# Performance work log

Hardware: AMD Instinct MI355X
Metric: run time of the kernel (lower is better)

Reference implementation:

```python
import jax, jax.numpy as jnp
import numpy as np
import math

L, Bt, IN, H = 512, 128, 512, 60


def setup_inputs() -> dict:
    key = jax.random.key(0)
    k1, k2, k3 = jax.random.split(key, 3)
    inp = jax.random.normal(k1, (L, Bt, IN), dtype=jnp.float32)
    W = jax.random.normal(k2, (H, IN), dtype=jnp.float32) / np.sqrt(IN)
    b = jnp.zeros((H,), dtype=jnp.float32)
    alphabet = jax.random.uniform(k3, (H, 3), dtype=jnp.float32, minval=-math.pi, maxval=math.pi)
    bond_lengths = jnp.array([132.868, 145.801, 152.326], dtype=jnp.float32)
    bond_angles = jnp.array([2.028, 2.124, 1.941], dtype=jnp.float32)
    return {"inp": inp, "W": W, "b": b, "alphabet": alphabet,
            "bond_lengths": bond_lengths, "bond_angles": bond_angles}


def reference(inp, W, b, alphabet, bond_lengths, bond_angles):
    Lr, Bb = inp.shape[0], inp.shape[1]
    # mixture over alphabet of torsion angles
    x = jax.nn.softmax(inp @ W.T + b, axis=2)                 # (L, B, H)
    phi = jnp.arctan2(x @ jnp.sin(alphabet), x @ jnp.cos(alphabet))  # (L, B, 3)
    # per residue i the loop consumes phi[i].T -> bond index is fastest axis
    phi_f = phi.transpose(0, 2, 1).reshape(Lr * 3, Bb)        # (3L, B)
    r = jnp.tile(bond_lengths, Lr)[:, None]                   # (3L, 1)
    th = jnp.tile(bond_angles, Lr)[:, None]                   # (3L, 1)
    # SRF coordinates of every new atom
    c_tilde = jnp.stack([
        (r * jnp.cos(th)) * jnp.ones_like(phi_f),
        r * jnp.cos(phi_f) * jnp.sin(th),
        r * jnp.sin(phi_f) * jnp.sin(th),
    ], axis=-1)                                               # (3L, B, 3)

    e = jnp.eye(3, dtype=inp.dtype)
    carry0 = (jnp.broadcast_to(e[0], (Bb, 3)),
              jnp.broadcast_to(e[1], (Bb, 3)),
              jnp.broadcast_to(e[2], (Bb, 3)))

    def step(carry, ct):
        A, Bp, C = carry                                      # each (B, 3)
        BC = C - Bp
        bc = BC / jnp.linalg.norm(BC, axis=1, keepdims=True)
        AB = Bp - A
        Nv = jnp.cross(AB, bc)
        n = Nv / jnp.linalg.norm(Nv, axis=1, keepdims=True)
        # D = C + R @ c_tilde, R columns = [bc, n x bc, n]
        D = C + bc * ct[:, 0:1] + jnp.cross(n, bc) * ct[:, 1:2] + n * ct[:, 2:3]
        return (Bp, C, D), D

    _, coords = jax.lax.scan(step, carry0, c_tilde)           # (3L, B, 3)
    return coords
```

## Files before the change

kernel.cpp:

```cpp
#include <hip/hip_runtime.h>
#include <math.h>

#define LSEQ  512
#define BT    128
#define INF   512
#define HH    60
#define NSTEP 1536
#define CH2   6

#define MTILE 64
#define KSTG  128
#define BROW  136

typedef __attribute__((ext_vector_type(8))) short bf16x8;
typedef __attribute__((ext_vector_type(4))) float floatx4;

__device__ __forceinline__ unsigned cvt_pk_bf16(float lo, float hi) {
  unsigned r;
  asm("v_cvt_pk_bf16_f32 %0, %1, %2" : "=v"(r) : "v"(lo), "v"(hi));
  return r;
}
__device__ __forceinline__ void split_pair(float a0, float a1,
                                           unsigned& hw, unsigned& lw) {
  hw = cvt_pk_bf16(a0, a1);
  float h0 = __uint_as_float(hw << 16);
  float h1 = __uint_as_float(hw & 0xFFFF0000u);
  lw = cvt_pk_bf16(a0 - h0, a1 - h1);
}

#define GLOAD(dst, ptr, voff) \
  asm volatile("global_load_dwordx4 %0, %1, %2" \
               : "=v"(dst) : "v"(voff), "s"(ptr))

#define WAIT_VM(n) \
  do { asm volatile("s_waitcnt vmcnt(" #n ")" ::: "memory"); \
       __builtin_amdgcn_sched_barrier(0); } while (0)

#define BARRIER() \
  do { asm volatile("s_waitcnt lgkmcnt(0)" ::: "memory"); \
       __builtin_amdgcn_s_barrier(); \
       asm volatile("" ::: "memory"); } while (0)


#define ISSUE_A(BUF, KB) \
  { _Pragma("unroll") \
    for (int ks_ = 0; ks_ < 4; ++ks_) { \
      GLOAD(BUF[2*ks_],   aBase + (KB) + ks_*32,     voffA); \
      GLOAD(BUF[2*ks_+1], aBase + (KB) + ks_*32 + 4, voffA); } }

#define ISSUE_W(KB) \
  { _Pragma("unroll") \
    for (int i_ = 0; i_ < 7; ++i_) \
      GLOAD(Wb[i_], W + (KB) + i_*4096, voffW); \
    GLOAD(Wb[7], W + (KB) + 7*4096, voffWc); }

#define SPLIT_W() \
  { _Pragma("unroll") \
    for (int i_ = 0; i_ < 8; ++i_) { \
      const int chunk_ = i_ * 256 + tid; \
      const int r_  = chunk_ >> 5; \
      const int j4_ = (chunk_ & 31) * 4; \
      floatx4 wv_ = Wb[i_]; \
      if (i_ == 7 && tid >= 128) wv_ = (floatx4){0.f, 0.f, 0.f, 0.f}; \
      unsigned h01_, l01_, h23_, l23_; \
      split_pair(wv_[0], wv_[1], h01_, l01_); \
      split_pair(wv_[2], wv_[3], h23_, l23_); \
      *(uint2*)&BhL[r_ * BROW + j4_] = make_uint2(h01_, h23_); \
      *(uint2*)&BlL[r_ * BROW + j4_] = make_uint2(l01_, l23_); } }

#define DO_STEPS(BUF) \
  { _Pragma("unroll") \
    for (int ks_ = 0; ks_ < 4; ++ks_) { \
      const int kl_ = ks_ * 32; \
      floatx4 x_ = BUF[2*ks_], y_ = BUF[2*ks_+1]; \
      uint4 uh_, ul_; \
      split_pair(x_[0], x_[1], uh_.x, ul_.x); \
      split_pair(x_[2], x_[3], uh_.y, ul_.y); \
      split_pair(y_[0], y_[1], uh_.z, ul_.z); \
      split_pair(y_[2], y_[3], uh_.w, ul_.w); \
      bf16x8 Ah_ = __builtin_bit_cast(bf16x8, uh_); \
      bf16x8 Al_ = __builtin_bit_cast(bf16x8, ul_); \
      _Pragma("unroll") \
      for (int nt_ = 0; nt_ < 4; ++nt_) { \
        const int boff_ = (nt_ * 16 + c) * BROW + kl_ + quad * 8; \
        bf16x8 Bh_ = *(const bf16x8*)&BhL[boff_]; \
        bf16x8 Bl_ = *(const bf16x8*)&BlL[boff_]; \
        acc[nt_] = __builtin_amdgcn_mfma_f32_16x16x32_bf16(Ah_, Bh_, acc[nt_], 0, 0, 0); \
        acc[nt_] = __builtin_amdgcn_mfma_f32_16x16x32_bf16(Ah_, Bl_, acc[nt_], 0, 0, 0); \
        acc[nt_] = __builtin_amdgcn_mfma_f32_16x16x32_bf16(Al_, Bh_, acc[nt_], 0, 0, 0); } } }

__global__ __launch_bounds__(256, 3) void k_phi(
    const float* __restrict__ inp, const float* __restrict__ W,
    const float* __restrict__ bias, const float* __restrict__ alphabet,
    float* __restrict__ phi_out) {
  __shared__ unsigned short BhL[64 * BROW];
  __shared__ unsigned short BlL[64 * BROW];
  __shared__ float sS[HH * 3], sC[HH * 3], sBias[64];

  const int tid  = threadIdx.x;
  const int lane = tid & 63;
  const int wid  = tid >> 6;
  const int c    = lane & 15;
  const int quad = lane >> 4;
  const int row0 = blockIdx.x * MTILE;

  if (tid < HH * 3) { float a = alphabet[tid]; sS[tid] = __sinf(a); sC[tid] = __cosf(a); }
  if (tid >= 192 && tid < 256) { int n = tid - 192; sBias[n] = (n < HH) ? bias[n] : 0.f; }

  floatx4 acc[4];
#pragma unroll
  for (int nt = 0; nt < 4; ++nt) acc[nt] = (floatx4){0.f, 0.f, 0.f, 0.f};

  const float* aBase = inp + (size_t)row0 * INF;
  const unsigned voffA  = ((unsigned)(wid * 16 + c) * INF + quad * 8) * 4u;
  const unsigned voffW  = ((unsigned)(tid >> 5) * INF + (tid & 31) * 4) * 4u;
  const unsigned voffWc = (tid < 128) ? voffW : 0u;

  floatx4 A0[8], A1[8], Wb[8];

  ISSUE_A(A0, 0);
  ISSUE_W(0);
  ISSUE_A(A1, KSTG);
  WAIT_VM(8);
  SPLIT_W();
  BARRIER();
  DO_STEPS(A0);
  BARRIER();

  ISSUE_W(KSTG);
  ISSUE_A(A0, 2 * KSTG);
  WAIT_VM(8);
  SPLIT_W();
  BARRIER();
  DO_STEPS(A1);
  BARRIER();

  ISSUE_W(2 * KSTG);
  ISSUE_A(A1, 3 * KSTG);
  WAIT_VM(8);
  SPLIT_W();
  BARRIER();
  DO_STEPS(A0);
  BARRIER();

  ISSUE_W(3 * KSTG);
  WAIT_VM(0);
  SPLIT_W();
  BARRIER();
  DO_STEPS(A1);

#pragma unroll
  for (int reg = 0; reg < 4; ++reg) {
    float lg[4];  bool val[4];
#pragma unroll
    for (int nt = 0; nt < 4; ++nt) {
      const int n = nt * 16 + c;
      val[nt] = (n < HH);
      lg[nt] = acc[nt][reg] + sBias[n];
    }
    float m = -1e30f;
#pragma unroll
    for (int nt = 0; nt < 4; ++nt) if (val[nt]) m = fmaxf(m, lg[nt]);
#pragma unroll
    for (int d = 1; d < 16; d <<= 1) m = fmaxf(m, __shfl_xor(m, d, 64));

    float s0=0.f,c0=0.f,s1=0.f,c1=0.f,s2=0.f,c2=0.f;
#pragma unroll
    for (int nt = 0; nt < 4; ++nt) {
      const int n = nt * 16 + c;
      float e = val[nt] ? __expf(lg[nt] - m) : 0.f;
      s0 = fmaf(e, sS[n*3+0], s0);  c0 = fmaf(e, sC[n*3+0], c0);
      s1 = fmaf(e, sS[n*3+1], s1);  c1 = fmaf(e, sC[n*3+1], c1);
      s2 = fmaf(e, sS[n*3+2], s2);  c2 = fmaf(e, sC[n*3+2], c2);
    }
#pragma unroll
    for (int d = 1; d < 16; d <<= 1) {
      s0 += __shfl_xor(s0, d, 64);  c0 += __shfl_xor(c0, d, 64);
      s1 += __shfl_xor(s1, d, 64);  c1 += __shfl_xor(c1, d, 64);
      s2 += __shfl_xor(s2, d, 64);  c2 += __shfl_xor(c2, d, 64);
    }
    if (c == 0) {
      const int row = row0 + wid * 16 + quad * 4 + reg;
      const int l  = row >> 7;
      const int bb = row & 127;
      float* pp = phi_out + (size_t)bb * NSTEP + 3 * l;
      pp[0] = atan2f(s0, c0);
      pp[1] = atan2f(s1, c1);
      pp[2] = atan2f(s2, c2);
    }
  }
}

struct Xf { float r[9]; float p[3]; };

__device__ __forceinline__ Xf compose(const Xf& A, const Xf& B) {
  Xf o;
#pragma unroll
  for (int i = 0; i < 3; ++i) {
#pragma unroll
    for (int j = 0; j < 3; ++j) {
      o.r[i*3+j] = fmaf(A.r[i*3+0], B.r[0+j],
                   fmaf(A.r[i*3+1], B.r[3+j],
                        A.r[i*3+2] * B.r[6+j]));
    }
    o.p[i] = fmaf(A.r[i*3+0], B.p[0],
             fmaf(A.r[i*3+1], B.p[1],
             fmaf(A.r[i*3+2], B.p[2], A.p[i])));
  }
  return o;
}

__device__ __forceinline__ Xf make_T(float phi, float st, float ct, float r) {
  float sp = __sinf(phi), cp = __cosf(phi);
  Xf T;
  T.r[0] = ct;      T.r[1] = -st;     T.r[2] = 0.f;
  T.r[3] = cp * st; T.r[4] = ct * cp; T.r[5] = -sp;
  T.r[6] = sp * st; T.r[7] = ct * sp; T.r[8] = cp;
  T.p[0] = r * ct;  T.p[1] = r * T.r[3]; T.p[2] = r * T.r[6];
  return T;
}

__device__ __forceinline__ void set_identity(Xf& X) {
  X.r[0]=1.f; X.r[1]=0.f; X.r[2]=0.f;
  X.r[3]=0.f; X.r[4]=1.f; X.r[5]=0.f;
  X.r[6]=0.f; X.r[7]=0.f; X.r[8]=1.f;
  X.p[0]=0.f; X.p[1]=0.f; X.p[2]=0.f;
}

__global__ __launch_bounds__(256) void k_scan(
    const float* __restrict__ phi, const float* __restrict__ bl,
    const float* __restrict__ ba, float* __restrict__ out) {
  __shared__ Xf wt[4];

  const int b = blockIdx.x;
  const int t = threadIdx.x & 63;
  const int w = threadIdx.x >> 6;
  const int g = threadIdx.x;

  float st[3], ct[3], rr[3];
#pragma unroll
  for (int j = 0; j < 3; ++j) {
    float a = ba[j];
    st[j] = __sinf(a); ct[j] = __cosf(a); rr[j] = bl[j];
  }

  float f[CH2];
  const float2* ph2 = (const float2*)(phi + (size_t)b * NSTEP + g * CH2);
#pragma unroll
  for (int q = 0; q < CH2/2; ++q) {
    float2 v = ph2[q];
    f[2*q+0] = v.x; f[2*q+1] = v.y;
  }

  Xf Q = make_T(f[0], st[0], ct[0], rr[0]);
#pragma unroll
  for (int s = 1; s < CH2; ++s)
    Q = compose(Q, make_T(f[s], st[s%3], ct[s%3], rr[s%3]));

#pragma unroll
  for (int d = 1; d < 64; d <<= 1) {
    Xf O;
#pragma unroll
    for (int q = 0; q < 9; ++q) O.r[q] = __shfl_up(Q.r[q], d, 64);
#pragma unroll
    for (int q = 0; q < 3; ++q) O.p[q] = __shfl_up(Q.p[q], d, 64);
    if (t < d) set_identity(O);
    Q = compose(O, Q);
  }

  if (t == 63) wt[w] = Q;
  __syncthreads();

  Xf E;
#pragma unroll
  for (int q = 0; q < 9; ++q) E.r[q] = __shfl_up(Q.r[q], 1, 64);
#pragma unroll
  for (int q = 0; q < 3; ++q) E.p[q] = __shfl_up(Q.p[q], 1, 64);
  if (t == 0) set_identity(E);

  Xf S0;
  S0.r[0] = 0.f;                  S0.r[1] = 0.816496580927726f;   S0.r[2] = 0.5773502691896258f;
  S0.r[3] = -0.7071067811865475f; S0.r[4] = -0.4082482904638631f; S0.r[5] = 0.5773502691896258f;
  S0.r[6] = 0.7071067811865475f;  S0.r[7] = -0.4082482904638631f; S0.r[8] = 0.5773502691896258f;
  S0.p[0] = 0.f; S0.p[1] = 0.f; S0.p[2] = 1.f;

  Xf SP = S0;
#pragma unroll
  for (int i = 0; i < 3; ++i)
    if (i < w) SP = compose(SP, wt[i]);

  Xf cur = compose(SP, E);

  float* op = out + (size_t)(g * CH2) * (BT * 3) + b * 3;
#pragma unroll
  for (int s = 0; s < CH2; ++s) {
    cur = compose(cur, make_T(f[s], st[s%3], ct[s%3], rr[s%3]));
    op[(size_t)s * (BT*3) + 0] = cur.p[0];
    op[(size_t)s * (BT*3) + 1] = cur.p[1];
    op[(size_t)s * (BT*3) + 2] = cur.p[2];
  }
}

extern "C" void kernel_launch(void* const* d_in, const int* in_sizes, int n_in,
                              void* d_out, int out_size, void* d_ws, size_t ws_size,
                              hipStream_t stream) {
  const float* inp      = (const float*)d_in[0];
  const float* W        = (const float*)d_in[1];
  const float* bias     = (const float*)d_in[2];
  const float* alphabet = (const float*)d_in[3];
  const float* bl       = (const float*)d_in[4];
  const float* ba       = (const float*)d_in[5];
  float* out = (float*)d_out;

  float* phi = (float*)d_ws;

  k_phi<<<dim3((LSEQ*BT)/MTILE), dim3(256), 0, stream>>>(inp, W, bias, alphabet, phi);
  k_scan<<<dim3(BT), dim3(256), 0, stream>>>(phi, bl, ba, out);
}
```

Measured before the change: 212.8 us.

## Replace double-buffered A stages with a five-slot per-k-step prefetch ring

The four coarse double-buffered A-tile stages in the projection GEMM are replaced by a rolling ring of five register slots, one per 32-wide k step. Each slot is refilled four steps ahead, with matching vmcnt waits. The next W tile load now starts right after the current one is split into LDS. The goal is to keep more global loads in flight, overlap them continuously with MFMA work, and lower peak register use. The cost is hand-tuned wait counts that must match the exact issue order, or the kernel reads stale registers.

```diff
diff --git a/kernel.cpp b/kernel.cpp
--- a/kernel.cpp
+++ b/kernel.cpp
@@ -42,11 +42,9 @@
        asm volatile("" ::: "memory"); } while (0)
 
 
-#define ISSUE_A(BUF, KB) \
-  { _Pragma("unroll") \
-    for (int ks_ = 0; ks_ < 4; ++ks_) { \
-      GLOAD(BUF[2*ks_],   aBase + (KB) + ks_*32,     voffA); \
-      GLOAD(BUF[2*ks_+1], aBase + (KB) + ks_*32 + 4, voffA); } }
+#define ISSUE_A_SLOT(J) \
+  { GLOAD(PF[(J) % 5][0], aBase + (J) * 32,     voffA); \
+    GLOAD(PF[(J) % 5][1], aBase + (J) * 32 + 4, voffA); }
 
 #define ISSUE_W(KB) \
   { _Pragma("unroll") \
@@ -68,27 +66,6 @@
       *(uint2*)&BhL[r_ * BROW + j4_] = make_uint2(h01_, h23_); \
       *(uint2*)&BlL[r_ * BROW + j4_] = make_uint2(l01_, l23_); } }
 
-#define DO_STEPS(BUF) \
-  { _Pragma("unroll") \
-    for (int ks_ = 0; ks_ < 4; ++ks_) { \
-      const int kl_ = ks_ * 32; \
-      floatx4 x_ = BUF[2*ks_], y_ = BUF[2*ks_+1]; \
-      uint4 uh_, ul_; \
-      split_pair(x_[0], x_[1], uh_.x, ul_.x); \
-      split_pair(x_[2], x_[3], uh_.y, ul_.y); \
-      split_pair(y_[0], y_[1], uh_.z, ul_.z); \
-      split_pair(y_[2], y_[3], uh_.w, ul_.w); \
-      bf16x8 Ah_ = __builtin_bit_cast(bf16x8, uh_); \
-      bf16x8 Al_ = __builtin_bit_cast(bf16x8, ul_); \
-      _Pragma("unroll") \
-      for (int nt_ = 0; nt_ < 4; ++nt_) { \
-        const int boff_ = (nt_ * 16 + c) * BROW + kl_ + quad * 8; \
-        bf16x8 Bh_ = *(const bf16x8*)&BhL[boff_]; \
-        bf16x8 Bl_ = *(const bf16x8*)&BlL[boff_]; \
-        acc[nt_] = __builtin_amdgcn_mfma_f32_16x16x32_bf16(Ah_, Bh_, acc[nt_], 0, 0, 0); \
-        acc[nt_] = __builtin_amdgcn_mfma_f32_16x16x32_bf16(Ah_, Bl_, acc[nt_], 0, 0, 0); \
-        acc[nt_] = __builtin_amdgcn_mfma_f32_16x16x32_bf16(Al_, Bh_, acc[nt_], 0, 0, 0); } } }
-
 __global__ __launch_bounds__(256, 3) void k_phi(
     const float* __restrict__ inp, const float* __restrict__ W,
     const float* __restrict__ bias, const float* __restrict__ alphabet,
@@ -116,38 +93,51 @@
   const unsigned voffW  = ((unsigned)(tid >> 5) * INF + (tid & 31) * 4) * 4u;
   const unsigned voffWc = (tid < 128) ? voffW : 0u;
 
-  floatx4 A0[8], A1[8], Wb[8];
-
-  ISSUE_A(A0, 0);
+  floatx4 PF[5][2];
+  floatx4 Wb[8];
+
   ISSUE_W(0);
-  ISSUE_A(A1, KSTG);
-  WAIT_VM(8);
-  SPLIT_W();
-  BARRIER();
-  DO_STEPS(A0);
-  BARRIER();
-
-  ISSUE_W(KSTG);
-  ISSUE_A(A0, 2 * KSTG);
-  WAIT_VM(8);
-  SPLIT_W();
-  BARRIER();
-  DO_STEPS(A1);
-  BARRIER();
-
-  ISSUE_W(2 * KSTG);
-  ISSUE_A(A1, 3 * KSTG);
-  WAIT_VM(8);
-  SPLIT_W();
-  BARRIER();
-  DO_STEPS(A0);
-  BARRIER();
-
-  ISSUE_W(3 * KSTG);
-  WAIT_VM(0);
-  SPLIT_W();
-  BARRIER();
-  DO_STEPS(A1);
+#pragma unroll
+  for (int j = 0; j < 4; ++j) ISSUE_A_SLOT(j);
+
+#pragma unroll
+  for (int s = 0; s < 4; ++s) {
+    WAIT_VM(8);
+    SPLIT_W();
+    if (s < 3) ISSUE_W((s + 1) * KSTG);
+    BARRIER();
+
+#pragma unroll
+    for (int t = 0; t < 4; ++t) {
+      const int j = s * 4 + t;
+      if (j + 4 < 16) ISSUE_A_SLOT(j + 4);
+      if (j <= 11)      WAIT_VM(16);
+      else if (j == 12) WAIT_VM(6);
+      else if (j == 13) WAIT_VM(4);
+      else if (j == 14) WAIT_VM(2);
+      else              WAIT_VM(0);
+
+      floatx4 x = PF[j % 5][0], y = PF[j % 5][1];
+      uint4 uh, ul;
+      split_pair(x[0], x[1], uh.x, ul.x);
+      split_pair(x[2], x[3], uh.y, ul.y);
+      split_pair(y[0], y[1], uh.z, ul.z);
+      split_pair(y[2], y[3], uh.w, ul.w);
+      bf16x8 Ah = __builtin_bit_cast(bf16x8, uh);
+      bf16x8 Al = __builtin_bit_cast(bf16x8, ul);
+      const int kl = t * 32;
+#pragma unroll
+      for (int nt = 0; nt < 4; ++nt) {
+        const int boff = (nt * 16 + c) * BROW + kl + quad * 8;
+        bf16x8 Bh = *(const bf16x8*)&BhL[boff];
+        bf16x8 Bl = *(const bf16x8*)&BlL[boff];
+        acc[nt] = __builtin_amdgcn_mfma_f32_16x16x32_bf16(Ah, Bh, acc[nt], 0, 0, 0);
+        acc[nt] = __builtin_amdgcn_mfma_f32_16x16x32_bf16(Ah, Bl, acc[nt], 0, 0, 0);
+        acc[nt] = __builtin_amdgcn_mfma_f32_16x16x32_bf16(Al, Bh, acc[nt], 0, 0, 0);
+      }
+    }
+    if (s < 3) BARRIER();
+  }
 
 #pragma unroll
   for (int reg = 0; reg < 4; ++reg) {
```

New measurement: 212.5 us. Within noise of the previous version (-0.2%).
